# Optimization experiments

Hardware: AMD Instinct MI355X
Metric: run time of the kernel (lower is better)

The kernel has to match this reference:

```python
import jax, jax.numpy as jnp
import numpy as np

B, F, D = 512, 128, 1024
EPS = 1e-5

def _ln(x, g, b):
    mu = jnp.mean(x, axis=-1, keepdims=True)
    var = jnp.mean(jnp.square(x - mu), axis=-1, keepdims=True)
    return (x - mu) * jax.lax.rsqrt(var + EPS) * g + b

def setup_inputs() -> dict:
    key = jax.random.key(0)
    ks = jax.random.split(key, 8)
    inp = {
        "text_embeds": jax.random.normal(ks[0], (B, D), jnp.float32),
        "video_embeds": jax.random.normal(ks[1], (B, F, D), jnp.float32),
    }
    # Linear weights: torch init is eye for all proj/linear layers; use small random
    # perturbation of identity to keep math non-trivial but realistic.
    def w(k):
        return jnp.eye(D, dtype=jnp.float32) + 0.02 * jax.random.normal(k, (D, D), jnp.float32)
    inp["q_w"], inp["k_w"], inp["v_w"] = w(ks[2]), w(ks[3]), w(ks[4])
    inp["out_w"], inp["lin_w"] = w(ks[5]), w(ks[6])
    for n in ("q_b", "k_b", "v_b", "out_b", "lin_b"):
        inp[n] = jnp.zeros((D,), jnp.float32)
    for i in (1, 2, 3):
        inp[f"ln{i}_g"] = jnp.ones((D,), jnp.float32)
        inp[f"ln{i}_b"] = jnp.zeros((D,), jnp.float32)
    return inp

def reference(text_embeds, video_embeds, q_w, k_w, v_w, out_w, lin_w,
              q_b, k_b, v_b, out_b, lin_b,
              ln1_g, ln1_b, ln2_g, ln2_b, ln3_g, ln3_b):
    t = _ln(text_embeds, ln1_g, ln1_b)                 # [B, D]
    vf = _ln(video_embeds, ln1_g, ln1_b)               # [B, F, D]
    q = t @ q_w.T + q_b                                # [B, D]
    k = vf @ k_w.T + k_b                               # [B, F, D]
    v = vf @ v_w.T + v_b                               # [B, F, D]
    logits = jnp.einsum("bd,bfd->bf", q, k) / jnp.sqrt(jnp.float32(D))
    w_att = jax.nn.softmax(logits, axis=-1)            # [B, F]
    attn = jnp.einsum("bf,bfd->bd", w_att, v)          # [B, D]
    attn = attn @ out_w.T + out_b
    attn_out = _ln(attn, ln2_g, ln2_b)
    linear_out = attn_out @ lin_w.T + lin_b
    # dropout: eval mode (identity)
    out = attn_out + linear_out
    return _ln(out, ln3_g, ln3_b)
```

## Files before the change

kernel.cpp:

```cpp
#include <hip/hip_runtime.h>

#define B_ 512
#define F_ 128
#define D_ 1024
#define EPS_ 1e-5f

typedef float f32x4 __attribute__((ext_vector_type(4)));
typedef __bf16 bf16x4 __attribute__((ext_vector_type(4)));
typedef __bf16 bf16x8 __attribute__((ext_vector_type(8)));

__global__ __launch_bounds__(256) void k_ln_f32(
    const float* __restrict__ X, const float* __restrict__ g,
    const float* __restrict__ bv, float* __restrict__ Y) {
  int row = blockIdx.x, t = threadIdx.x;
  f32x4 xv = *(const f32x4*)(X + (size_t)row * D_ + t * 4);
  float s = xv[0] + xv[1] + xv[2] + xv[3];
  float ss = xv[0] * xv[0] + xv[1] * xv[1] + xv[2] * xv[2] + xv[3] * xv[3];
  __shared__ float r1[256], r2[256];
  r1[t] = s; r2[t] = ss;
  __syncthreads();
  for (int o = 128; o > 0; o >>= 1) {
    if (t < o) { r1[t] += r1[t + o]; r2[t] += r2[t + o]; }
    __syncthreads();
  }
  float mu = r1[0] * (1.0f / D_);
  float var = r2[0] * (1.0f / D_) - mu * mu;
  float rs = rsqrtf(var + EPS_);
  f32x4 gg = *(const f32x4*)(g + t * 4);
  f32x4 bb = *(const f32x4*)(bv + t * 4);
  f32x4 o4;
  o4[0] = (xv[0] - mu) * rs * gg[0] + bb[0];
  o4[1] = (xv[1] - mu) * rs * gg[1] + bb[1];
  o4[2] = (xv[2] - mu) * rs * gg[2] + bb[2];
  o4[3] = (xv[3] - mu) * rs * gg[3] + bb[3];
  *(f32x4*)(Y + (size_t)row * D_ + t * 4) = o4;
}

__global__ __launch_bounds__(256) void k_final(
    const float* __restrict__ X1, const float* __restrict__ X2,
    const float* __restrict__ g, const float* __restrict__ bv,
    float* __restrict__ out) {
  int row = blockIdx.x, t = threadIdx.x;
  f32x4 a = *(const f32x4*)(X1 + (size_t)row * D_ + t * 4);
  f32x4 b = *(const f32x4*)(X2 + (size_t)row * D_ + t * 4);
  float v0 = a[0] + b[0], v1 = a[1] + b[1], v2 = a[2] + b[2], v3 = a[3] + b[3];
  float s = v0 + v1 + v2 + v3;
  float ss = v0 * v0 + v1 * v1 + v2 * v2 + v3 * v3;
  __shared__ float r1[256], r2[256];
  r1[t] = s; r2[t] = ss;
  __syncthreads();
  for (int o = 128; o > 0; o >>= 1) {
    if (t < o) { r1[t] += r1[t + o]; r2[t] += r2[t + o]; }
    __syncthreads();
  }
  float mu = r1[0] * (1.0f / D_);
  float var = r2[0] * (1.0f / D_) - mu * mu;
  float rs = rsqrtf(var + EPS_);
  f32x4 gg = *(const f32x4*)(g + t * 4);
  f32x4 bb = *(const f32x4*)(bv + t * 4);
  f32x4 o4;
  o4[0] = (v0 - mu) * rs * gg[0] + bb[0];
  o4[1] = (v1 - mu) * rs * gg[1] + bb[1];
  o4[2] = (v2 - mu) * rs * gg[2] + bb[2];
  o4[3] = (v3 - mu) * rs * gg[3] + bb[3];
  *(f32x4*)(out + (size_t)row * D_ + t * 4) = o4;
}

__global__ __launch_bounds__(256) void k_wprep(
    const float* __restrict__ w0, const float* __restrict__ w1,
    const float* __restrict__ w2, const float* __restrict__ w3,
    const float* __restrict__ w4, __bf16* __restrict__ o0,
    __bf16* __restrict__ o1, __bf16* __restrict__ o2,
    __bf16* __restrict__ o3, __bf16* __restrict__ o4p) {
  int z = blockIdx.z;
  const float* src = (z == 0) ? w0 : (z == 1) ? w1 : (z == 2) ? w2 : (z == 3) ? w3 : w4;
  __bf16* dst = (z == 0) ? o0 : (z == 1) ? o1 : (z == 2) ? o2 : (z == 3) ? o3 : o4p;
  int t = threadIdx.x;
  if (z != 1) {
    int row = blockIdx.y * 32 + (t >> 3);
    int col = blockIdx.x * 32 + (t & 7) * 4;
    f32x4 v = *(const f32x4*)(src + (size_t)row * D_ + col);
    bf16x4 o;
    o[0] = (__bf16)v[0]; o[1] = (__bf16)v[1]; o[2] = (__bf16)v[2]; o[3] = (__bf16)v[3];
    *(bf16x4*)(dst + (size_t)row * D_ + col) = o;
  } else {
    __shared__ float tile[32][33];
    int ti = blockIdx.y, tj = blockIdx.x;
    int c = t & 31, r0 = t >> 5;
#pragma unroll
    for (int i = 0; i < 4; i++) {
      int r = r0 + i * 8;
      tile[r][c] = src[(size_t)(ti * 32 + r) * D_ + tj * 32 + c];
    }
    __syncthreads();
#pragma unroll
    for (int i = 0; i < 4; i++) {
      int r = r0 + i * 8;
      dst[(size_t)(tj * 32 + r) * D_ + ti * 32 + c] = (__bf16)tile[c][r];
    }
  }
}

__global__ __launch_bounds__(64) void k_gemm32(
    const float* __restrict__ A, const __bf16* __restrict__ W,
    const float* __restrict__ bias, float* __restrict__ C, int N, int K) {
  int lane = threadIdx.x;
  int r = lane & 15, quad = lane >> 4;
  int tn = blockIdx.x, tm = blockIdx.y;
  const float* pa0 = A + (size_t)(tm * 32 + r) * K + quad * 8;
  const float* pa1 = pa0 + (size_t)16 * K;
  const __bf16* pw0 = W + (size_t)(tn * 32 + r) * K + quad * 8;
  const __bf16* pw1 = pw0 + (size_t)16 * K;
  f32x4 acc00 = {0,0,0,0}, acc01 = {0,0,0,0}, acc10 = {0,0,0,0}, acc11 = {0,0,0,0};
  f32x4 a0lo = *(const f32x4*)(pa0);
  f32x4 a0hi = *(const f32x4*)(pa0 + 4);
  f32x4 a1lo = *(const f32x4*)(pa1);
  f32x4 a1hi = *(const f32x4*)(pa1 + 4);
  bf16x8 w0v = *(const bf16x8*)(pw0);
  bf16x8 w1v = *(const bf16x8*)(pw1);
  for (int k0 = 0; k0 < K; k0 += 32) {
    int kn = (k0 + 32 < K) ? (k0 + 32) : 0;
    f32x4 na0lo = *(const f32x4*)(pa0 + kn);
    f32x4 na0hi = *(const f32x4*)(pa0 + kn + 4);
    f32x4 na1lo = *(const f32x4*)(pa1 + kn);
    f32x4 na1hi = *(const f32x4*)(pa1 + kn + 4);
    bf16x8 nw0 = *(const bf16x8*)(pw0 + kn);
    bf16x8 nw1 = *(const bf16x8*)(pw1 + kn);
    bf16x8 ah0, al0, ah1, al1;
#pragma unroll
    for (int i = 0; i < 4; i++) {
      float v = a0lo[i];
      ah0[i] = (__bf16)v; al0[i] = (__bf16)(v - (float)ah0[i]);
      v = a0hi[i];
      ah0[i+4] = (__bf16)v; al0[i+4] = (__bf16)(v - (float)ah0[i+4]);
      v = a1lo[i];
      ah1[i] = (__bf16)v; al1[i] = (__bf16)(v - (float)ah1[i]);
      v = a1hi[i];
      ah1[i+4] = (__bf16)v; al1[i+4] = (__bf16)(v - (float)ah1[i+4]);
    }
    acc00 = __builtin_amdgcn_mfma_f32_16x16x32_bf16(ah0, w0v, acc00, 0, 0, 0);
    acc00 = __builtin_amdgcn_mfma_f32_16x16x32_bf16(al0, w0v, acc00, 0, 0, 0);
    acc01 = __builtin_amdgcn_mfma_f32_16x16x32_bf16(ah0, w1v, acc01, 0, 0, 0);
    acc01 = __builtin_amdgcn_mfma_f32_16x16x32_bf16(al0, w1v, acc01, 0, 0, 0);
    acc10 = __builtin_amdgcn_mfma_f32_16x16x32_bf16(ah1, w0v, acc10, 0, 0, 0);
    acc10 = __builtin_amdgcn_mfma_f32_16x16x32_bf16(al1, w0v, acc10, 0, 0, 0);
    acc11 = __builtin_amdgcn_mfma_f32_16x16x32_bf16(ah1, w1v, acc11, 0, 0, 0);
    acc11 = __builtin_amdgcn_mfma_f32_16x16x32_bf16(al1, w1v, acc11, 0, 0, 0);
    a0lo = na0lo; a0hi = na0hi; a1lo = na1lo; a1hi = na1hi;
    w0v = nw0; w1v = nw1;
  }
  int col0 = tn * 32 + r, col1 = col0 + 16;
  float b0 = bias ? bias[col0] : 0.0f;
  float b1 = bias ? bias[col1] : 0.0f;
  int row0 = tm * 32 + quad * 4;
#pragma unroll
  for (int i = 0; i < 4; i++) {
    C[(size_t)(row0 + i) * N + col0] = acc00[i] + b0;
    C[(size_t)(row0 + i) * N + col1] = acc01[i] + b1;
    C[(size_t)(row0 + 16 + i) * N + col0] = acc10[i] + b0;
    C[(size_t)(row0 + 16 + i) * N + col1] = acc11[i] + b1;
  }
}

__global__ __launch_bounds__(256) void k_prep_q(
    const float* __restrict__ q2, const float* __restrict__ q,
    const float* __restrict__ g, const float* __restrict__ bv,
    const float* __restrict__ kb, float* __restrict__ gq,
    float* __restrict__ sum_gq, float* __restrict__ dot_bq, float* __restrict__ qkb) {
  int b = blockIdx.x, t = threadIdx.x;
  f32x4 q2v = *(const f32x4*)(q2 + (size_t)b * D_ + t * 4);
  f32x4 qv = *(const f32x4*)(q + (size_t)b * D_ + t * 4);
  f32x4 gg = *(const f32x4*)(g + t * 4);
  f32x4 bb = *(const f32x4*)(bv + t * 4);
  f32x4 kk = *(const f32x4*)(kb + t * 4);
  f32x4 gqv;
  gqv[0] = gg[0] * q2v[0]; gqv[1] = gg[1] * q2v[1];
  gqv[2] = gg[2] * q2v[2]; gqv[3] = gg[3] * q2v[3];
  *(f32x4*)(gq + (size_t)b * D_ + t * 4) = gqv;
  float s1 = gqv[0] + gqv[1] + gqv[2] + gqv[3];
  float s2 = bb[0] * q2v[0] + bb[1] * q2v[1] + bb[2] * q2v[2] + bb[3] * q2v[3];
  float s3 = kk[0] * qv[0] + kk[1] * qv[1] + kk[2] * qv[2] + kk[3] * qv[3];
  __shared__ float r1[256], r2[256], r3[256];
  r1[t] = s1; r2[t] = s2; r3[t] = s3;
  __syncthreads();
  for (int o = 128; o > 0; o >>= 1) {
    if (t < o) { r1[t] += r1[t + o]; r2[t] += r2[t + o]; r3[t] += r3[t + o]; }
    __syncthreads();
  }
  if (t == 0) { sum_gq[b] = r1[0]; dot_bq[b] = r2[0]; qkb[b] = r3[0]; }
}

__global__ __launch_bounds__(1024) void k_attn(
    const float* __restrict__ video, const float* __restrict__ gq,
    const float* __restrict__ sum_gq, const float* __restrict__ dot_bq,
    const float* __restrict__ qkb, const float* __restrict__ g,
    const float* __restrict__ bv, float* __restrict__ ctx) {
  __shared__ float X[32][D_];
  __shared__ float l_s[32], mu_s[32], rs_s[32], a_s[32];
  __shared__ float alpha_s, S_s, C_s;
  int b = blockIdx.x, t = threadIdx.x;
  int row = t >> 5, c = t & 31;
  const float* vbase = video + ((size_t)b * F_ + row) * D_ + c * 32;
  f32x4 gqr[8];
  const float* gp = gq + (size_t)b * D_ + c * 32;
#pragma unroll
  for (int i = 0; i < 8; i++) gqr[i] = *(const f32x4*)(gp + i * 4);
  float sgq = sum_gq[b], dbq = dot_bq[b], qk = qkb[b];
  f32x4 vr[8];
#pragma unroll
  for (int i = 0; i < 8; i++) vr[i] = *(const f32x4*)(vbase + i * 4);
  float O = 0.0f;
  float m_run = -1e30f, S = 0.0f, Cc = 0.0f;
  for (int T = 0; T < 4; T++) {
    float sx = 0.f, sxx = 0.f, sxg = 0.f;
#pragma unroll
    for (int i = 0; i < 8; i++) {
      f32x4 v = vr[i];
      sx += v[0] + v[1] + v[2] + v[3];
      sxx += v[0]*v[0] + v[1]*v[1] + v[2]*v[2] + v[3]*v[3];
      f32x4 gg = gqr[i];
      sxg += v[0]*gg[0] + v[1]*gg[1] + v[2]*gg[2] + v[3]*gg[3];
      *(f32x4*)(&X[row][c * 32 + i * 4]) = v;
    }
#pragma unroll
    for (int o = 16; o > 0; o >>= 1) {
      sx += __shfl_xor(sx, o);
      sxx += __shfl_xor(sxx, o);
      sxg += __shfl_xor(sxg, o);
    }
    if (c == 0) {
      float mu = sx * (1.0f / D_);
      float var = sxx * (1.0f / D_) - mu * mu;
      float rs = rsqrtf(var + EPS_);
      l_s[row] = (rs * (sxg - mu * sgq) + dbq + qk) * 0.03125f;
      mu_s[row] = mu; rs_s[row] = rs;
    }
    if (T < 3) {
      const float* nb = vbase + (size_t)(T + 1) * 32 * D_;
#pragma unroll
      for (int i = 0; i < 8; i++) vr[i] = *(const f32x4*)(nb + i * 4);
    }
    __syncthreads();
    if (t < 32) {
      float lf = l_s[t], mt = lf;
#pragma unroll
      for (int o = 16; o > 0; o >>= 1) mt = fmaxf(mt, __shfl_xor(mt, o));
      float m_new = fmaxf(m_run, mt);
      float alpha = __expf(m_run - m_new);
      float e = __expf(lf - m_new);
      float af = e * rs_s[t];
      a_s[t] = af;
      float se = e, sc = af * mu_s[t];
#pragma unroll
      for (int o = 16; o > 0; o >>= 1) {
        se += __shfl_xor(se, o);
        sc += __shfl_xor(sc, o);
      }
      S = S * alpha + se;
      Cc = Cc * alpha + sc;
      m_run = m_new;
      if (t == 0) { alpha_s = alpha; S_s = S; C_s = Cc; }
    }
    __syncthreads();
    float alpha = alpha_s;
    float acc = 0.0f;
#pragma unroll
    for (int fi = 0; fi < 32; fi++) acc += a_s[fi] * X[fi][t];
    O = O * alpha + acc;
    if (T < 3) __syncthreads();
  }
  float inv = 1.0f / S_s;
  ctx[(size_t)b * D_ + t] = g[t] * ((O - C_s) * inv) + bv[t];
}

extern "C" void kernel_launch(void* const* d_in, const int* in_sizes, int n_in,
                              void* d_out, int out_size, void* d_ws, size_t ws_size,
                              hipStream_t stream) {
  (void)in_sizes; (void)n_in; (void)out_size; (void)ws_size;
  const float* text = (const float*)d_in[0];
  const float* video = (const float*)d_in[1];
  const float* q_w = (const float*)d_in[2];
  const float* k_w = (const float*)d_in[3];
  const float* v_w = (const float*)d_in[4];
  const float* out_w = (const float*)d_in[5];
  const float* lin_w = (const float*)d_in[6];
  const float* q_b = (const float*)d_in[7];
  const float* k_b = (const float*)d_in[8];
  const float* v_b = (const float*)d_in[9];
  const float* out_b = (const float*)d_in[10];
  const float* lin_b = (const float*)d_in[11];
  const float* ln1_g = (const float*)d_in[12];
  const float* ln1_b = (const float*)d_in[13];
  const float* ln2_g = (const float*)d_in[14];
  const float* ln2_b = (const float*)d_in[15];
  const float* ln3_g = (const float*)d_in[16];
  const float* ln3_b = (const float*)d_in[17];
  float* out = (float*)d_out;

  const size_t BD = (size_t)B_ * D_;
  const size_t DD = (size_t)D_ * D_;
  float* f = (float*)d_ws;
  float* slotA = f;
  float* slotB = f + BD;
  float* slotC = f + 2 * BD;
  float* sum_gq = f + 3 * BD;
  float* dot_bq = sum_gq + B_;
  float* qkb = sum_gq + 2 * B_;
  __bf16* Wq = (__bf16*)(sum_gq + 4 * B_);
  __bf16* WkT = Wq + DD;
  __bf16* Wv = Wq + 2 * DD;
  __bf16* Wo = Wq + 3 * DD;
  __bf16* Wl = Wq + 4 * DD;

  dim3 gemm_grid(D_ / 32, B_ / 32);

  k_wprep<<<dim3(32, 32, 5), 256, 0, stream>>>(q_w, k_w, v_w, out_w, lin_w,
                                               Wq, WkT, Wv, Wo, Wl);
  k_ln_f32<<<B_, 256, 0, stream>>>(text, ln1_g, ln1_b, slotA);
  k_gemm32<<<gemm_grid, 64, 0, stream>>>(slotA, Wq, q_b, slotB, D_, D_);
  k_gemm32<<<gemm_grid, 64, 0, stream>>>(slotB, WkT, nullptr, slotA, D_, D_);
  k_prep_q<<<B_, 256, 0, stream>>>(slotA, slotB, ln1_g, ln1_b, k_b, slotC,
                                   sum_gq, dot_bq, qkb);
  k_attn<<<B_, 1024, 0, stream>>>(video, slotC, sum_gq, dot_bq, qkb,
                                  ln1_g, ln1_b, slotA);
  k_gemm32<<<gemm_grid, 64, 0, stream>>>(slotA, Wv, v_b, slotB, D_, D_);
  k_gemm32<<<gemm_grid, 64, 0, stream>>>(slotB, Wo, out_b, slotA, D_, D_);
  k_ln_f32<<<B_, 256, 0, stream>>>(slotA, ln2_g, ln2_b, slotC);
  k_gemm32<<<gemm_grid, 64, 0, stream>>>(slotC, Wl, lin_b, slotA, D_, D_);
  k_final<<<B_, 256, 0, stream>>>(slotC, slotA, ln3_g, ln3_b, out);
}
```

Measured before the change: 556.4 us.

## Store GEMM activations as pre-split bf16 hi/lo pairs and use shuffle reductions

GEMM A operands are now produced by the preceding kernel (layernorm, GEMM epilogue, attention) as bf16 high and low halves, so the GEMM inner loop no longer converts fp32 to split bf16 on every K step. The MFMA order is regrouped so all high-part products issue before the low-part ones. Block reductions in the layernorm, final and prep kernels switch from a shared-memory tree with many barriers to wavefront shuffles. The attention kernel's video loads become lane-strided for coalescing, and its shared tile is padded. Activation traffic per element stays the same (two bf16 vs one fp32), but the conversion work moves out of the K loop.

```diff
diff --git a/kernel.cpp b/kernel.cpp
--- a/kernel.cpp
+++ b/kernel.cpp
@@ -9,60 +9,74 @@
 typedef __bf16 bf16x4 __attribute__((ext_vector_type(4)));
 typedef __bf16 bf16x8 __attribute__((ext_vector_type(8)));
 
-__global__ __launch_bounds__(256) void k_ln_f32(
+template <int OUT>
+__global__ __launch_bounds__(256) void k_ln(
     const float* __restrict__ X, const float* __restrict__ g,
-    const float* __restrict__ bv, float* __restrict__ Y) {
+    const float* __restrict__ bv, float* __restrict__ Yf,
+    __bf16* __restrict__ Yh, __bf16* __restrict__ Yl) {
   int row = blockIdx.x, t = threadIdx.x;
   f32x4 xv = *(const f32x4*)(X + (size_t)row * D_ + t * 4);
   float s = xv[0] + xv[1] + xv[2] + xv[3];
   float ss = xv[0] * xv[0] + xv[1] * xv[1] + xv[2] * xv[2] + xv[3] * xv[3];
-  __shared__ float r1[256], r2[256];
-  r1[t] = s; r2[t] = ss;
+#pragma unroll
+  for (int o = 32; o > 0; o >>= 1) { s += __shfl_xor(s, o); ss += __shfl_xor(ss, o); }
+  __shared__ float ws[4][2];
+  int w = t >> 6;
+  if ((t & 63) == 0) { ws[w][0] = s; ws[w][1] = ss; }
   __syncthreads();
-  for (int o = 128; o > 0; o >>= 1) {
-    if (t < o) { r1[t] += r1[t + o]; r2[t] += r2[t + o]; }
-    __syncthreads();
-  }
-  float mu = r1[0] * (1.0f / D_);
-  float var = r2[0] * (1.0f / D_) - mu * mu;
+  s = ws[0][0] + ws[1][0] + ws[2][0] + ws[3][0];
+  ss = ws[0][1] + ws[1][1] + ws[2][1] + ws[3][1];
+  float mu = s * (1.0f / D_);
+  float var = ss * (1.0f / D_) - mu * mu;
   float rs = rsqrtf(var + EPS_);
   f32x4 gg = *(const f32x4*)(g + t * 4);
   f32x4 bb = *(const f32x4*)(bv + t * 4);
   f32x4 o4;
-  o4[0] = (xv[0] - mu) * rs * gg[0] + bb[0];
-  o4[1] = (xv[1] - mu) * rs * gg[1] + bb[1];
-  o4[2] = (xv[2] - mu) * rs * gg[2] + bb[2];
-  o4[3] = (xv[3] - mu) * rs * gg[3] + bb[3];
-  *(f32x4*)(Y + (size_t)row * D_ + t * 4) = o4;
+#pragma unroll
+  for (int i = 0; i < 4; i++) o4[i] = (xv[i] - mu) * rs * gg[i] + bb[i];
+  if (OUT == 0) {
+    *(f32x4*)(Yf + (size_t)row * D_ + t * 4) = o4;
+  } else {
+    bf16x4 h4, l4;
+#pragma unroll
+    for (int i = 0; i < 4; i++) {
+      h4[i] = (__bf16)o4[i];
+      l4[i] = (__bf16)(o4[i] - (float)h4[i]);
+    }
+    *(bf16x4*)(Yh + (size_t)row * D_ + t * 4) = h4;
+    *(bf16x4*)(Yl + (size_t)row * D_ + t * 4) = l4;
+  }
 }
 
 __global__ __launch_bounds__(256) void k_final(
-    const float* __restrict__ X1, const float* __restrict__ X2,
-    const float* __restrict__ g, const float* __restrict__ bv,
-    float* __restrict__ out) {
+    const __bf16* __restrict__ X1h, const __bf16* __restrict__ X1l,
+    const float* __restrict__ X2, const float* __restrict__ g,
+    const float* __restrict__ bv, float* __restrict__ out) {
   int row = blockIdx.x, t = threadIdx.x;
-  f32x4 a = *(const f32x4*)(X1 + (size_t)row * D_ + t * 4);
+  bf16x4 h4 = *(const bf16x4*)(X1h + (size_t)row * D_ + t * 4);
+  bf16x4 l4 = *(const bf16x4*)(X1l + (size_t)row * D_ + t * 4);
   f32x4 b = *(const f32x4*)(X2 + (size_t)row * D_ + t * 4);
-  float v0 = a[0] + b[0], v1 = a[1] + b[1], v2 = a[2] + b[2], v3 = a[3] + b[3];
-  float s = v0 + v1 + v2 + v3;
-  float ss = v0 * v0 + v1 * v1 + v2 * v2 + v3 * v3;
-  __shared__ float r1[256], r2[256];
-  r1[t] = s; r2[t] = ss;
+  f32x4 v;
+#pragma unroll
+  for (int i = 0; i < 4; i++) v[i] = (float)h4[i] + (float)l4[i] + b[i];
+  float s = v[0] + v[1] + v[2] + v[3];
+  float ss = v[0] * v[0] + v[1] * v[1] + v[2] * v[2] + v[3] * v[3];
+#pragma unroll
+  for (int o = 32; o > 0; o >>= 1) { s += __shfl_xor(s, o); ss += __shfl_xor(ss, o); }
+  __shared__ float ws[4][2];
+  int w = t >> 6;
+  if ((t & 63) == 0) { ws[w][0] = s; ws[w][1] = ss; }
   __syncthreads();
-  for (int o = 128; o > 0; o >>= 1) {
-    if (t < o) { r1[t] += r1[t + o]; r2[t] += r2[t + o]; }
-    __syncthreads();
-  }
-  float mu = r1[0] * (1.0f / D_);
-  float var = r2[0] * (1.0f / D_) - mu * mu;
+  s = ws[0][0] + ws[1][0] + ws[2][0] + ws[3][0];
+  ss = ws[0][1] + ws[1][1] + ws[2][1] + ws[3][1];
+  float mu = s * (1.0f / D_);
+  float var = ss * (1.0f / D_) - mu * mu;
   float rs = rsqrtf(var + EPS_);
   f32x4 gg = *(const f32x4*)(g + t * 4);
   f32x4 bb = *(const f32x4*)(bv + t * 4);
   f32x4 o4;
-  o4[0] = (v0 - mu) * rs * gg[0] + bb[0];
-  o4[1] = (v1 - mu) * rs * gg[1] + bb[1];
-  o4[2] = (v2 - mu) * rs * gg[2] + bb[2];
-  o4[3] = (v3 - mu) * rs * gg[3] + bb[3];
+#pragma unroll
+  for (int i = 0; i < 4; i++) o4[i] = (v[i] - mu) * rs * gg[i] + bb[i];
   *(f32x4*)(out + (size_t)row * D_ + t * 4) = o4;
 }
 
@@ -101,53 +115,42 @@
   }
 }
 
+template <int OUT>
 __global__ __launch_bounds__(64) void k_gemm32(
-    const float* __restrict__ A, const __bf16* __restrict__ W,
-    const float* __restrict__ bias, float* __restrict__ C, int N, int K) {
+    const __bf16* __restrict__ Ah, const __bf16* __restrict__ Al,
+    const __bf16* __restrict__ W, const float* __restrict__ bias,
+    float* __restrict__ Cf, __bf16* __restrict__ Ch, __bf16* __restrict__ Cl,
+    int N, int K) {
   int lane = threadIdx.x;
   int r = lane & 15, quad = lane >> 4;
   int tn = blockIdx.x, tm = blockIdx.y;
-  const float* pa0 = A + (size_t)(tm * 32 + r) * K + quad * 8;
-  const float* pa1 = pa0 + (size_t)16 * K;
+  const __bf16* pah0 = Ah + (size_t)(tm * 32 + r) * K + quad * 8;
+  const __bf16* pah1 = pah0 + (size_t)16 * K;
+  const __bf16* pal0 = Al + (size_t)(tm * 32 + r) * K + quad * 8;
+  const __bf16* pal1 = pal0 + (size_t)16 * K;
   const __bf16* pw0 = W + (size_t)(tn * 32 + r) * K + quad * 8;
   const __bf16* pw1 = pw0 + (size_t)16 * K;
   f32x4 acc00 = {0,0,0,0}, acc01 = {0,0,0,0}, acc10 = {0,0,0,0}, acc11 = {0,0,0,0};
-  f32x4 a0lo = *(const f32x4*)(pa0);
-  f32x4 a0hi = *(const f32x4*)(pa0 + 4);
-  f32x4 a1lo = *(const f32x4*)(pa1);
-  f32x4 a1hi = *(const f32x4*)(pa1 + 4);
-  bf16x8 w0v = *(const bf16x8*)(pw0);
-  bf16x8 w1v = *(const bf16x8*)(pw1);
+  bf16x8 ah0 = *(const bf16x8*)pah0, ah1 = *(const bf16x8*)pah1;
+  bf16x8 al0 = *(const bf16x8*)pal0, al1 = *(const bf16x8*)pal1;
+  bf16x8 w0v = *(const bf16x8*)pw0, w1v = *(const bf16x8*)pw1;
   for (int k0 = 0; k0 < K; k0 += 32) {
     int kn = (k0 + 32 < K) ? (k0 + 32) : 0;
-    f32x4 na0lo = *(const f32x4*)(pa0 + kn);
-    f32x4 na0hi = *(const f32x4*)(pa0 + kn + 4);
-    f32x4 na1lo = *(const f32x4*)(pa1 + kn);
-    f32x4 na1hi = *(const f32x4*)(pa1 + kn + 4);
+    bf16x8 nah0 = *(const bf16x8*)(pah0 + kn);
+    bf16x8 nah1 = *(const bf16x8*)(pah1 + kn);
+    bf16x8 nal0 = *(const bf16x8*)(pal0 + kn);
+    bf16x8 nal1 = *(const bf16x8*)(pal1 + kn);
     bf16x8 nw0 = *(const bf16x8*)(pw0 + kn);
     bf16x8 nw1 = *(const bf16x8*)(pw1 + kn);
-    bf16x8 ah0, al0, ah1, al1;
-#pragma unroll
-    for (int i = 0; i < 4; i++) {
-      float v = a0lo[i];
-      ah0[i] = (__bf16)v; al0[i] = (__bf16)(v - (float)ah0[i]);
-      v = a0hi[i];
-      ah0[i+4] = (__bf16)v; al0[i+4] = (__bf16)(v - (float)ah0[i+4]);
-      v = a1lo[i];
-      ah1[i] = (__bf16)v; al1[i] = (__bf16)(v - (float)ah1[i]);
-      v = a1hi[i];
-      ah1[i+4] = (__bf16)v; al1[i+4] = (__bf16)(v - (float)ah1[i+4]);
-    }
     acc00 = __builtin_amdgcn_mfma_f32_16x16x32_bf16(ah0, w0v, acc00, 0, 0, 0);
+    acc01 = __builtin_amdgcn_mfma_f32_16x16x32_bf16(ah0, w1v, acc01, 0, 0, 0);
+    acc10 = __builtin_amdgcn_mfma_f32_16x16x32_bf16(ah1, w0v, acc10, 0, 0, 0);
+    acc11 = __builtin_amdgcn_mfma_f32_16x16x32_bf16(ah1, w1v, acc11, 0, 0, 0);
     acc00 = __builtin_amdgcn_mfma_f32_16x16x32_bf16(al0, w0v, acc00, 0, 0, 0);
-    acc01 = __builtin_amdgcn_mfma_f32_16x16x32_bf16(ah0, w1v, acc01, 0, 0, 0);
     acc01 = __builtin_amdgcn_mfma_f32_16x16x32_bf16(al0, w1v, acc01, 0, 0, 0);
-    acc10 = __builtin_amdgcn_mfma_f32_16x16x32_bf16(ah1, w0v, acc10, 0, 0, 0);
     acc10 = __builtin_amdgcn_mfma_f32_16x16x32_bf16(al1, w0v, acc10, 0, 0, 0);
-    acc11 = __builtin_amdgcn_mfma_f32_16x16x32_bf16(ah1, w1v, acc11, 0, 0, 0);
     acc11 = __builtin_amdgcn_mfma_f32_16x16x32_bf16(al1, w1v, acc11, 0, 0, 0);
-    a0lo = na0lo; a0hi = na0hi; a1lo = na1lo; a1hi = na1hi;
-    w0v = nw0; w1v = nw1;
+    ah0 = nah0; ah1 = nah1; al0 = nal0; al1 = nal1; w0v = nw0; w1v = nw1;
   }
   int col0 = tn * 32 + r, col1 = col0 + 16;
   float b0 = bias ? bias[col0] : 0.0f;
@@ -155,60 +158,81 @@
   int row0 = tm * 32 + quad * 4;
 #pragma unroll
   for (int i = 0; i < 4; i++) {
-    C[(size_t)(row0 + i) * N + col0] = acc00[i] + b0;
-    C[(size_t)(row0 + i) * N + col1] = acc01[i] + b1;
-    C[(size_t)(row0 + 16 + i) * N + col0] = acc10[i] + b0;
-    C[(size_t)(row0 + 16 + i) * N + col1] = acc11[i] + b1;
+    float v00 = acc00[i] + b0, v01 = acc01[i] + b1;
+    float v10 = acc10[i] + b0, v11 = acc11[i] + b1;
+    size_t o00 = (size_t)(row0 + i) * N + col0, o01 = (size_t)(row0 + i) * N + col1;
+    size_t o10 = (size_t)(row0 + 16 + i) * N + col0, o11 = (size_t)(row0 + 16 + i) * N + col1;
+    if (OUT == 0) {
+      Cf[o00] = v00; Cf[o01] = v01; Cf[o10] = v10; Cf[o11] = v11;
+    } else {
+      __bf16 h;
+      h = (__bf16)v00; Ch[o00] = h; Cl[o00] = (__bf16)(v00 - (float)h);
+      h = (__bf16)v01; Ch[o01] = h; Cl[o01] = (__bf16)(v01 - (float)h);
+      h = (__bf16)v10; Ch[o10] = h; Cl[o10] = (__bf16)(v10 - (float)h);
+      h = (__bf16)v11; Ch[o11] = h; Cl[o11] = (__bf16)(v11 - (float)h);
+    }
   }
 }
 
 __global__ __launch_bounds__(256) void k_prep_q(
-    const float* __restrict__ q2, const float* __restrict__ q,
-    const float* __restrict__ g, const float* __restrict__ bv,
-    const float* __restrict__ kb, float* __restrict__ gq,
-    float* __restrict__ sum_gq, float* __restrict__ dot_bq, float* __restrict__ qkb) {
+    const float* __restrict__ q2, const __bf16* __restrict__ qh,
+    const __bf16* __restrict__ ql, const float* __restrict__ g,
+    const float* __restrict__ bv, const float* __restrict__ kb,
+    float* __restrict__ gq, float* __restrict__ sum_gq,
+    float* __restrict__ dot_bq, float* __restrict__ qkb) {
   int b = blockIdx.x, t = threadIdx.x;
   f32x4 q2v = *(const f32x4*)(q2 + (size_t)b * D_ + t * 4);
-  f32x4 qv = *(const f32x4*)(q + (size_t)b * D_ + t * 4);
+  bf16x4 h4 = *(const bf16x4*)(qh + (size_t)b * D_ + t * 4);
+  bf16x4 l4 = *(const bf16x4*)(ql + (size_t)b * D_ + t * 4);
   f32x4 gg = *(const f32x4*)(g + t * 4);
   f32x4 bb = *(const f32x4*)(bv + t * 4);
   f32x4 kk = *(const f32x4*)(kb + t * 4);
   f32x4 gqv;
-  gqv[0] = gg[0] * q2v[0]; gqv[1] = gg[1] * q2v[1];
-  gqv[2] = gg[2] * q2v[2]; gqv[3] = gg[3] * q2v[3];
+  float s1 = 0.f, s2 = 0.f, s3 = 0.f;
+#pragma unroll
+  for (int i = 0; i < 4; i++) {
+    gqv[i] = gg[i] * q2v[i];
+    s1 += gqv[i];
+    s2 += bb[i] * q2v[i];
+    s3 += kk[i] * ((float)h4[i] + (float)l4[i]);
+  }
   *(f32x4*)(gq + (size_t)b * D_ + t * 4) = gqv;
-  float s1 = gqv[0] + gqv[1] + gqv[2] + gqv[3];
-  float s2 = bb[0] * q2v[0] + bb[1] * q2v[1] + bb[2] * q2v[2] + bb[3] * q2v[3];
-  float s3 = kk[0] * qv[0] + kk[1] * qv[1] + kk[2] * qv[2] + kk[3] * qv[3];
-  __shared__ float r1[256], r2[256], r3[256];
-  r1[t] = s1; r2[t] = s2; r3[t] = s3;
+#pragma unroll
+  for (int o = 32; o > 0; o >>= 1) {
+    s1 += __shfl_xor(s1, o); s2 += __shfl_xor(s2, o); s3 += __shfl_xor(s3, o);
+  }
+  __shared__ float ws[4][3];
+  int w = t >> 6;
+  if ((t & 63) == 0) { ws[w][0] = s1; ws[w][1] = s2; ws[w][2] = s3; }
   __syncthreads();
-  for (int o = 128; o > 0; o >>= 1) {
-    if (t < o) { r1[t] += r1[t + o]; r2[t] += r2[t + o]; r3[t] += r3[t + o]; }
-    __syncthreads();
-  }
-  if (t == 0) { sum_gq[b] = r1[0]; dot_bq[b] = r2[0]; qkb[b] = r3[0]; }
-}
-
+  if (t == 0) {
+    sum_gq[b] = ws[0][0] + ws[1][0] + ws[2][0] + ws[3][0];
+    dot_bq[b] = ws[0][1] + ws[1][1] + ws[2][1] + ws[3][1];
+    qkb[b] = ws[0][2] + ws[1][2] + ws[2][2] + ws[3][2];
+  }
+}
+
+#define XPAD 1032
 __global__ __launch_bounds__(1024) void k_attn(
     const float* __restrict__ video, const float* __restrict__ gq,
     const float* __restrict__ sum_gq, const float* __restrict__ dot_bq,
     const float* __restrict__ qkb, const float* __restrict__ g,
-    const float* __restrict__ bv, float* __restrict__ ctx) {
-  __shared__ float X[32][D_];
+    const float* __restrict__ bv, __bf16* __restrict__ ctxh,
+    __bf16* __restrict__ ctxl) {
+  __shared__ float X[32][XPAD];
   __shared__ float l_s[32], mu_s[32], rs_s[32], a_s[32];
   __shared__ float alpha_s, S_s, C_s;
   int b = blockIdx.x, t = threadIdx.x;
   int row = t >> 5, c = t & 31;
-  const float* vbase = video + ((size_t)b * F_ + row) * D_ + c * 32;
+  const float* vbase = video + ((size_t)b * F_ + row) * D_ + c * 4;
   f32x4 gqr[8];
-  const float* gp = gq + (size_t)b * D_ + c * 32;
-#pragma unroll
-  for (int i = 0; i < 8; i++) gqr[i] = *(const f32x4*)(gp + i * 4);
+  const float* gp = gq + (size_t)b * D_ + c * 4;
+#pragma unroll
+  for (int i = 0; i < 8; i++) gqr[i] = *(const f32x4*)(gp + i * 128);
   float sgq = sum_gq[b], dbq = dot_bq[b], qk = qkb[b];
   f32x4 vr[8];
 #pragma unroll
-  for (int i = 0; i < 8; i++) vr[i] = *(const f32x4*)(vbase + i * 4);
+  for (int i = 0; i < 8; i++) vr[i] = *(const f32x4*)(vbase + i * 128);
   float O = 0.0f;
   float m_run = -1e30f, S = 0.0f, Cc = 0.0f;
   for (int T = 0; T < 4; T++) {
@@ -220,7 +244,7 @@
       sxx += v[0]*v[0] + v[1]*v[1] + v[2]*v[2] + v[3]*v[3];
       f32x4 gg = gqr[i];
       sxg += v[0]*gg[0] + v[1]*gg[1] + v[2]*gg[2] + v[3]*gg[3];
-      *(f32x4*)(&X[row][c * 32 + i * 4]) = v;
+      *(f32x4*)(&X[row][c * 4 + i * 128]) = v;
     }
 #pragma unroll
     for (int o = 16; o > 0; o >>= 1) {
@@ -238,7 +262,7 @@
     if (T < 3) {
       const float* nb = vbase + (size_t)(T + 1) * 32 * D_;
 #pragma unroll
-      for (int i = 0; i < 8; i++) vr[i] = *(const f32x4*)(nb + i * 4);
+      for (int i = 0; i < 8; i++) vr[i] = *(const f32x4*)(nb + i * 128);
     }
     __syncthreads();
     if (t < 32) {
@@ -270,7 +294,10 @@
     if (T < 3) __syncthreads();
   }
   float inv = 1.0f / S_s;
-  ctx[(size_t)b * D_ + t] = g[t] * ((O - C_s) * inv) + bv[t];
+  float v = g[t] * ((O - C_s) * inv) + bv[t];
+  __bf16 h = (__bf16)v;
+  ctxh[(size_t)b * D_ + t] = h;
+  ctxl[(size_t)b * D_ + t] = (__bf16)(v - (float)h);
 }
 
 extern "C" void kernel_launch(void* const* d_in, const int* in_sizes, int n_in,
@@ -300,13 +327,18 @@
   const size_t BD = (size_t)B_ * D_;
   const size_t DD = (size_t)D_ * D_;
   float* f = (float*)d_ws;
-  float* slotA = f;
-  float* slotB = f + BD;
-  float* slotC = f + 2 * BD;
-  float* sum_gq = f + 3 * BD;
+  float* slotF1 = f;
+  float* slotF2 = f + BD;
+  float* sum_gq = f + 2 * BD;
   float* dot_bq = sum_gq + B_;
   float* qkb = sum_gq + 2 * B_;
-  __bf16* Wq = (__bf16*)(sum_gq + 4 * B_);
+  __bf16* P1h = (__bf16*)(sum_gq + 4 * B_);
+  __bf16* P1l = P1h + BD;
+  __bf16* P2h = P1h + 2 * BD;
+  __bf16* P2l = P1h + 3 * BD;
+  __bf16* P3h = P1h + 4 * BD;
+  __bf16* P3l = P1h + 5 * BD;
+  __bf16* Wq = P1h + 6 * BD;
   __bf16* WkT = Wq + DD;
   __bf16* Wv = Wq + 2 * DD;
   __bf16* Wo = Wq + 3 * DD;
@@ -316,16 +348,16 @@
 
   k_wprep<<<dim3(32, 32, 5), 256, 0, stream>>>(q_w, k_w, v_w, out_w, lin_w,
                                                Wq, WkT, Wv, Wo, Wl);
-  k_ln_f32<<<B_, 256, 0, stream>>>(text, ln1_g, ln1_b, slotA);
-  k_gemm32<<<gemm_grid, 64, 0, stream>>>(slotA, Wq, q_b, slotB, D_, D_);
-  k_gemm32<<<gemm_grid, 64, 0, stream>>>(slotB, WkT, nullptr, slotA, D_, D_);
-  k_prep_q<<<B_, 256, 0, stream>>>(slotA, slotB, ln1_g, ln1_b, k_b, slotC,
-                                   sum_gq, dot_bq, qkb);
-  k_attn<<<B_, 1024, 0, stream>>>(video, slotC, sum_gq, dot_bq, qkb,
-                                  ln1_g, ln1_b, slotA);
-  k_gemm32<<<gemm_grid, 64, 0, stream>>>(slotA, Wv, v_b, slotB, D_, D_);
-  k_gemm32<<<gemm_grid, 64, 0, stream>>>(slotB, Wo, out_b, slotA, D_, D_);
-  k_ln_f32<<<B_, 256, 0, stream>>>(slotA, ln2_g, ln2_b, slotC);
-  k_gemm32<<<gemm_grid, 64, 0, stream>>>(slotC, Wl, lin_b, slotA, D_, D_);
-  k_final<<<B_, 256, 0, stream>>>(slotC, slotA, ln3_g, ln3_b, out);
-}
+  k_ln<1><<<B_, 256, 0, stream>>>(text, ln1_g, ln1_b, nullptr, P1h, P1l);
+  k_gemm32<1><<<gemm_grid, 64, 0, stream>>>(P1h, P1l, Wq, q_b, nullptr, P2h, P2l, D_, D_);
+  k_gemm32<0><<<gemm_grid, 64, 0, stream>>>(P2h, P2l, WkT, nullptr, slotF1, nullptr, nullptr, D_, D_);
+  k_prep_q<<<B_, 256, 0, stream>>>(slotF1, P2h, P2l, ln1_g, ln1_b, k_b,
+                                   slotF2, sum_gq, dot_bq, qkb);
+  k_attn<<<B_, 1024, 0, stream>>>(video, slotF2, sum_gq, dot_bq, qkb,
+                                  ln1_g, ln1_b, P1h, P1l);
+  k_gemm32<1><<<gemm_grid, 64, 0, stream>>>(P1h, P1l, Wv, v_b, nullptr, P2h, P2l, D_, D_);
+  k_gemm32<0><<<gemm_grid, 64, 0, stream>>>(P2h, P2l, Wo, out_b, slotF1, nullptr, nullptr, D_, D_);
+  k_ln<1><<<B_, 256, 0, stream>>>(slotF1, ln2_g, ln2_b, nullptr, P3h, P3l);
+  k_gemm32<0><<<gemm_grid, 64, 0, stream>>>(P3h, P3l, Wl, lin_b, slotF2, nullptr, nullptr, D_, D_);
+  k_final<<<B_, 256, 0, stream>>>(P3h, P3l, slotF2, ln3_g, ln3_b, out);
+}
```

New measurement: 523.4 us. 5.9% less time.
